# Performance work log

Hardware: AMD Instinct MI355X
Metric: run time of the kernel (lower is better)

The kernel has to match this reference:

```python
import jax, jax.numpy as jnp
import numpy as np

S, B, H, N = 512, 32, 512, 131072  # seq_len, batch, hidden_dim, num candidate spans
MAX_STEP = 20  # max_length


def setup_inputs() -> dict:
    key = jax.random.key(0)
    ks = jax.random.split(key, 8)
    hidden = jax.random.normal(ks[0], (S, B, 2 * H), dtype=jnp.float32)
    span_bids = jax.random.randint(ks[1], (N,), 0, B, dtype=jnp.int32)
    # begin in [1, S-1-MAX_STEP-1] so that begin-1>=0 and end=begin+step <= S-1
    span_begins = jax.random.randint(ks[2], (N,), 1, S - MAX_STEP - 2, dtype=jnp.int32)
    steps = jax.random.randint(ks[3], (N,), 2, MAX_STEP + 1, dtype=jnp.int32)
    span_ends = span_begins + steps
    span_flags = jax.random.randint(ks[4], (N,), 0, 2, dtype=jnp.int32)
    span_weights = jax.random.uniform(ks[5], (N,), dtype=jnp.float32)
    W1 = jax.random.normal(ks[6], (2 * H, H), dtype=jnp.float32) / np.sqrt(2.0 * H)
    b1 = jnp.zeros((H,), dtype=jnp.float32)
    W2 = jax.random.normal(ks[7], (H, 1), dtype=jnp.float32) / np.sqrt(float(H))
    b2 = jnp.zeros((1,), dtype=jnp.float32)
    return {"hidden": hidden, "span_bids": span_bids, "span_begins": span_begins,
            "span_ends": span_ends, "span_flags": span_flags, "span_weights": span_weights,
            "W1": W1, "b1": b1, "W2": W2, "b2": b2}


def reference(hidden, span_bids, span_begins, span_ends, span_flags, span_weights, W1, b1, W2, b2):
    h = W2.shape[0]  # hidden_dim
    # vectorized _span_embed: fwd diff on first half, bwd diff on second half
    fwd = hidden[span_ends - 1, span_bids, :h] - hidden[span_begins - 1, span_bids, :h]
    bwd = hidden[span_begins, span_bids, h:] - hidden[span_ends, span_bids, h:]
    feats = jnp.concatenate([fwd, bwd], axis=-1)  # [N, 2H]
    z = jnp.maximum(feats @ W1 + b1, 0.0)
    p = jax.nn.sigmoid(z @ W2 + b2)[:, 0]  # [N]
    targets = (span_flags == 1).astype(p.dtype)
    n_pos = jnp.sum(targets)
    n_tot = jnp.asarray(targets.shape[0], p.dtype)
    scale = 2.0 * n_pos / n_tot  # negative weights scaled by 2*P/(P+N)
    w_eff = jnp.where(span_flags == 1, span_weights, span_weights * scale)
    pc = jnp.clip(p, 1e-7, 1.0 - 1e-7)
    bce = -(targets * jnp.log(pc) + (1.0 - targets) * jnp.log(1.0 - pc))
    loss = jnp.mean(w_eff * bce)
    return loss
```

## Files before the change

kernel.cpp:

```cpp
#include <hip/hip_runtime.h>
#include <hip/hip_bf16.h>


typedef float f32x4 __attribute__((ext_vector_type(4)));
typedef float f32x2 __attribute__((ext_vector_type(2)));
typedef __bf16 bf16x8 __attribute__((ext_vector_type(8)));
typedef __bf16 bf16x4 __attribute__((ext_vector_type(4)));

__device__ __forceinline__ unsigned short f2bf(float f) {
  unsigned int u = __float_as_uint(f);
  u += 0x7fffu + ((u >> 16) & 1u);
  return (unsigned short)(u >> 16);
}
__device__ __forceinline__ float bf2f(unsigned int lo16) {
  return __uint_as_float(lo16 << 16);
}

__global__ void prep(const float* __restrict__ W1,
                     unsigned short* __restrict__ W1b,
                     const int* __restrict__ bids, int* __restrict__ ghist,
                     int nspans) {
  __shared__ int h[32];
  int t = threadIdx.x;
  if (blockIdx.x < 256) {
    int idx = blockIdx.x * 256 + t;
    int kc = idx & 3;
    int n  = (idx >> 2) & 511;
    int c  = idx >> 11;
    int k0 = c * 32 + kc * 8;
    unsigned short tmp[8];
#pragma unroll
    for (int j = 0; j < 8; ++j)
      tmp[j] = f2bf(W1[(k0 + j) * 512 + n]);
    *(uint4*)(W1b + c * 16384 + n * 32 + kc * 8) = *(uint4*)tmp;
  } else {
    if (t < 32) h[t] = 0;
    __syncthreads();
    int base = (blockIdx.x - 256) * 1024;
#pragma unroll
    for (int i = 0; i < 4; ++i) {
      int idx = base + t + i * 256;
      if (idx < nspans) atomicAdd(&h[bids[idx]], 1);
    }
    __syncthreads();
    if (t < 32) atomicAdd(&ghist[t], h[t]);
  }
}

__global__ void span_scatter(const int* __restrict__ bids,
                             const int* __restrict__ ghist,
                             int* __restrict__ gslot,
                             int* __restrict__ sidx, int nspans) {
  __shared__ int lh[32], lbase[32], lcur[32];
  int t = threadIdx.x;
  if (t < 32) lh[t] = 0;
  __syncthreads();
  int base = blockIdx.x * 512;
  int myb[2];
#pragma unroll
  for (int i = 0; i < 2; ++i) {
    int idx = base + t + i * 256;
    myb[i] = (idx < nspans) ? bids[idx] : -1;
    if (myb[i] >= 0) atomicAdd(&lh[myb[i]], 1);
  }
  __syncthreads();
  if (t < 32) {
    int pre = 0;
    for (int j = 0; j < t; ++j) pre += ghist[j];
    lbase[t] = pre + atomicAdd(&gslot[t], lh[t]);
    lcur[t] = 0;
  }
  __syncthreads();
#pragma unroll
  for (int i = 0; i < 2; ++i) {
    int b = myb[i];
    if (b >= 0) {
      int pos = lbase[b] + atomicAdd(&lcur[b], 1);
      sidx[pos] = base + t + i * 256;
    }
  }
}

__global__ __launch_bounds__(512, 4) void proj_gemm(
    const float* __restrict__ hidden,
    const unsigned short* __restrict__ w1b,
    unsigned char* __restrict__ Wq) {
  __shared__ __align__(16) unsigned short LB[32768];

  const int t = threadIdx.x;
  const int lane = t & 63;
  const int w = t >> 6;
  const int r0 = blockIdx.x << 6;
  const int hk = blockIdx.y << 9;
  const int q = lane >> 4;
  const int m = lane & 15;

  {
    const int kq = lane >> 4;
    const int sm = lane & 15;
#pragma unroll
    for (int ii = 0; ii < 2; ++ii) {
      const int it = (w << 1) + ii;
#pragma unroll
      for (int mt = 0; mt < 4; ++mt) {
#pragma unroll
        for (int hh = 0; hh < 2; ++hh) {
          const int kk_ = (hh << 4) + (kq << 2);
          const float* gp = hidden + ((r0 + (mt << 4) + sm) << 10)
                                   + hk + (it << 5) + kk_;
          float4 f = *(const float4*)gp;
          bf16x4 hv;
          hv[0] = (__bf16)f.x; hv[1] = (__bf16)f.y;
          hv[2] = (__bf16)f.z; hv[3] = (__bf16)f.w;
          const int qq = kk_ >> 3;
          const int kkr = kk_ & 7;
          *(bf16x4*)(LB + (((it << 2) + mt) << 9)
                        + (((qq << 4) + sm) << 3) + kkr) = hv;
        }
      }
    }
  }
  __syncthreads();

  int boffn[4];
#pragma unroll
  for (int nt = 0; nt < 4; ++nt)
    boffn[nt] = (((w << 6) + (nt << 4) + m) << 5) + (q << 3);
  const unsigned short* w1base = w1b + (blockIdx.y << 18);

  f32x4 acc[4][4];
#pragma unroll
  for (int i = 0; i < 4; ++i)
#pragma unroll
    for (int j = 0; j < 4; ++j) acc[i][j] = (f32x4){0.f, 0.f, 0.f, 0.f};

#pragma unroll
  for (int it = 0; it < 16; ++it) {
    const unsigned short* bt = w1base + (it << 14);
    bf16x8 bfr[4];
#pragma unroll
    for (int nt = 0; nt < 4; ++nt)
      bfr[nt] = *(const bf16x8*)(bt + boffn[nt]);
    bf16x8 af[4];
#pragma unroll
    for (int mt = 0; mt < 4; ++mt)
      af[mt] = *(const bf16x8*)(LB + (((it << 2) + mt) << 9)
                                   + (((q << 4) + m) << 3));
#pragma unroll
    for (int mt = 0; mt < 4; ++mt)
#pragma unroll
      for (int nt = 0; nt < 4; ++nt)
        acc[mt][nt] = __builtin_amdgcn_mfma_f32_16x16x32_bf16(af[mt], bfr[nt],
                                                              acc[mt][nt], 0, 0, 0);
  }

  {
    const int cb = (w << 6) + (m << 2);
#pragma unroll
    for (int mt = 0; mt < 4; ++mt) {
#pragma unroll
      for (int r = 0; r < 4; ++r) {
        unsigned int o = __builtin_amdgcn_cvt_pk_fp8_f32(
            acc[mt][0][r], acc[mt][1][r], 0, false);
        o = __builtin_amdgcn_cvt_pk_fp8_f32(
            acc[mt][2][r], acc[mt][3][r], o, true);
        int grow = r0 + (mt << 4) + (q << 2) + r;
        if (hk == 0) {
          *(unsigned int*)(Wq + (grow << 10) + cb) = o;
        } else if (grow >= 32) {
          *(unsigned int*)(Wq + ((grow - 32) << 10) + 512 + cb) = o;
        }
      }
    }
  }
}

#define SPB 64
__global__ __launch_bounds__(256) void span_eval(
    const unsigned char* __restrict__ Wq,
    const int* __restrict__ sidx,
    const int* __restrict__ bids, const int* __restrict__ begins,
    const int* __restrict__ ends, const int* __restrict__ flags,
    const float* __restrict__ weights,
    const float* __restrict__ b1, const float* __restrict__ w2,
    const float* __restrict__ b2, float* __restrict__ partials) {
  __shared__ int oB[SPB], oE[SPB], sfl[SPB];
  __shared__ float swt[SPB];
  __shared__ float red[4][3];
  const int t = threadIdx.x;
  const int lane = t & 63;
  const int w = t >> 6;
  const int h = lane >> 5;
  const int hl = lane & 31;

  const int nblk = gridDim.x;
  int lb = blockIdx.x;
  if ((nblk & 7) == 0) {
    const int cpx = nblk >> 3;
    lb = (blockIdx.x & 7) * cpx + (blockIdx.x >> 3);
  }
  const int sbase = lb * SPB;

  if (t < SPB) {
    int s = sidx[sbase + t];
    int b = bids[s], bg = begins[s], en = ends[s];
    oB[t] = (((bg - 1) << 5) + b) << 10;
    oE[t] = (((en - 1) << 5) + b) << 10;
    sfl[t] = flags[s];
    swt[t] = weights[s];
  }
  __syncthreads();

  const int sp0 = ((w << 1) + h) << 3;
  const int c0 = hl << 4;
  f32x2 b1p[8], w2p[8];
#pragma unroll
  for (int i = 0; i < 8; ++i) {
#pragma unroll
    for (int j2 = 0; j2 < 2; ++j2) {
      int j = 2 * i + j2;
      int colp = ((hl >> 2) << 6) + ((j & 3) << 4) + ((hl & 3) << 2) + (j >> 2);
      b1p[i][j2] = b1[colp];
      w2p[i][j2] = w2[colp];
    }
  }

  auto dec2 = [](unsigned int v, f32x2* f) {
    f[0] = __builtin_amdgcn_cvt_pk_f32_fp8(v, false);
    f[1] = __builtin_amdgcn_cvt_pk_f32_fp8(v, true);
  };

  uint4 BU[4], BV[4], EU[4], EV[4];
  auto ld = [&](int slot, int j) {
    int ob = oB[sp0 + j], oe = oE[sp0 + j];
    BU[slot] = *(const uint4*)(Wq + ob + c0);
    BV[slot] = *(const uint4*)(Wq + ob + 512 + c0);
    EU[slot] = *(const uint4*)(Wq + oe + c0);
    EV[slot] = *(const uint4*)(Wq + oe + 512 + c0);
  };
  ld(0, 0); ld(1, 1); ld(2, 2); ld(3, 3);

  const f32x2 zero2 = (f32x2){0.f, 0.f};
  float mylogit = 0.f;
#pragma unroll
  for (int j = 0; j < 8; ++j) {
    const int slot = j & 3;
    f32x2 bu2[8], bv2[8], eu2[8], ev2[8];
    dec2(BU[slot].x, bu2 + 0); dec2(BU[slot].y, bu2 + 2);
    dec2(BU[slot].z, bu2 + 4); dec2(BU[slot].w, bu2 + 6);
    dec2(BV[slot].x, bv2 + 0); dec2(BV[slot].y, bv2 + 2);
    dec2(BV[slot].z, bv2 + 4); dec2(BV[slot].w, bv2 + 6);
    dec2(EU[slot].x, eu2 + 0); dec2(EU[slot].y, eu2 + 2);
    dec2(EU[slot].z, eu2 + 4); dec2(EU[slot].w, eu2 + 6);
    dec2(EV[slot].x, ev2 + 0); dec2(EV[slot].y, ev2 + 2);
    dec2(EV[slot].z, ev2 + 4); dec2(EV[slot].w, ev2 + 6);
    if (j + 4 < 8) ld(slot, j + 4);
    f32x2 sv2 = zero2;
#pragma unroll
    for (int i = 0; i < 8; ++i) {
      f32x2 zp = eu2[i] - bu2[i] + bv2[i] - ev2[i] + b1p[i];
      zp = __builtin_elementwise_max(zp, zero2);
      sv2 = sv2 + zp * w2p[i];
    }
    float sv = sv2[0] + sv2[1];
    sv += __shfl_xor(sv, 1);
    sv += __shfl_xor(sv, 2);
    sv += __shfl_xor(sv, 4);
    sv += __shfl_xor(sv, 8);
    sv += __shfl_xor(sv, 16);
    if (hl == j) mylogit = sv;
  }

  mylogit = __shfl(mylogit, ((lane & 8) << 2) + (lane & 7));

  float pos_t = 0.f, neg_t = 0.f, cnt_t = 0.f;
  if (lane < 16) {
    int sl = (w << 4) + lane;
    float logit = mylogit + b2[0];
    float p = 1.f / (1.f + expf(-logit));
    p = fminf(fmaxf(p, 1e-7f), 1.f - 1e-7f);
    int fl = sfl[sl];
    float bce = (fl == 1) ? -logf(p) : -logf(1.f - p);
    float term = swt[sl] * bce;
    pos_t = (fl == 1) ? term : 0.f;
    neg_t = (fl == 1) ? 0.f : term;
    cnt_t = (fl == 1) ? 1.f : 0.f;
  }
#pragma unroll
  for (int off = 1; off < 64; off <<= 1) {
    pos_t += __shfl_xor(pos_t, off);
    neg_t += __shfl_xor(neg_t, off);
    cnt_t += __shfl_xor(cnt_t, off);
  }
  if (lane == 0) { red[w][0] = pos_t; red[w][1] = neg_t; red[w][2] = cnt_t; }
  __syncthreads();
  if (t == 0) {
    partials[(blockIdx.x << 2) + 0] = red[0][0] + red[1][0] + red[2][0] + red[3][0];
    partials[(blockIdx.x << 2) + 1] = red[0][1] + red[1][1] + red[2][1] + red[3][1];
    partials[(blockIdx.x << 2) + 2] = red[0][2] + red[1][2] + red[2][2] + red[3][2];
  }
}

__global__ void finalize(const float* __restrict__ parts, int nblk,
                         float* __restrict__ out, int nspans) {
  __shared__ float sp[4], sn[4], sc[4];
  float P = 0.f, Ng = 0.f, C = 0.f;
  for (int i = threadIdx.x; i < nblk; i += 256) {
    P += parts[(i << 2) + 0];
    Ng += parts[(i << 2) + 1];
    C += parts[(i << 2) + 2];
  }
#pragma unroll
  for (int off = 1; off < 64; off <<= 1) {
    P += __shfl_xor(P, off);
    Ng += __shfl_xor(Ng, off);
    C += __shfl_xor(C, off);
  }
  int w = threadIdx.x >> 6;
  if ((threadIdx.x & 63) == 0) { sp[w] = P; sn[w] = Ng; sc[w] = C; }
  __syncthreads();
  if (threadIdx.x == 0) {
    P = sp[0] + sp[1] + sp[2] + sp[3];
    Ng = sn[0] + sn[1] + sn[2] + sn[3];
    C = sc[0] + sc[1] + sc[2] + sc[3];
    float scale = 2.f * C / (float)nspans;
    out[0] = (P + scale * Ng) / (float)nspans;
  }
}

extern "C" void kernel_launch(void* const* d_in, const int* in_sizes, int n_in,
                              void* d_out, int out_size, void* d_ws, size_t ws_size,
                              hipStream_t stream) {
  const float* hidden = (const float*)d_in[0];
  const int* bids     = (const int*)d_in[1];
  const int* begins   = (const int*)d_in[2];
  const int* ends     = (const int*)d_in[3];
  const int* flags    = (const int*)d_in[4];
  const float* weights = (const float*)d_in[5];
  const float* W1 = (const float*)d_in[6];
  const float* b1 = (const float*)d_in[7];
  const float* W2 = (const float*)d_in[8];
  const float* b2 = (const float*)d_in[9];
  float* out = (float*)d_out;
  const int nspans = in_sizes[1];
  const int nblk = nspans / SPB;

  float* partials = (float*)d_ws;
  unsigned short* W1b = (unsigned short*)((char*)d_ws + (1 << 18));
  unsigned char* Wq = (unsigned char*)((char*)d_ws + (2 << 20));
  int* ghist = (int*)((char*)d_ws + (19 << 20));
  int* gslot = ghist + 32;
  int* sidx  = (int*)((char*)d_ws + (20 << 20));

  hipMemsetAsync(ghist, 0, 64 * sizeof(int), stream);
  prep<<<384, 256, 0, stream>>>(W1, W1b, bids, ghist, nspans);
  span_scatter<<<(nspans + 511) / 512, 256, 0, stream>>>(bids, ghist, gslot,
                                                         sidx, nspans);
  proj_gemm<<<dim3(256, 2), 512, 0, stream>>>(hidden, W1b, Wq);
  span_eval<<<nblk, 256, 0, stream>>>(Wq, sidx, bids, begins, ends, flags,
                                      weights, b1, W2, b2, partials);
  finalize<<<1, 256, 0, stream>>>(partials, nblk, out, nspans);
}
```

Baseline: 166.2 us.

## Process four span chunks per block with double-buffered span metadata

span_eval now loops over four 64-span chunks per block instead of one, so the grid shrinks fourfold. The per-span setup (b1/w2 loads, b2 read, the block reduction and partial write) is amortised across the chunks. Metadata for the next chunk is loaded into a second shared buffer while the current chunk's gathers run. This cuts per-block overhead and the finalize input size, at the cost of fewer blocks to hide gather latency and an extra barrier per chunk.

```diff
diff --git a/kernel.cpp b/kernel.cpp
--- a/kernel.cpp
+++ b/kernel.cpp
@@ -176,6 +176,7 @@
 }
 
 #define SPB 64
+#define CHUNKS 4
 __global__ __launch_bounds__(256) void span_eval(
     const unsigned char* __restrict__ Wq,
     const int* __restrict__ sidx,
@@ -184,8 +185,8 @@
     const float* __restrict__ weights,
     const float* __restrict__ b1, const float* __restrict__ w2,
     const float* __restrict__ b2, float* __restrict__ partials) {
-  __shared__ int oB[SPB], oE[SPB], sfl[SPB];
-  __shared__ float swt[SPB];
+  __shared__ int oB[2][SPB], oE[2][SPB], sfl[2][SPB];
+  __shared__ float swt[2][SPB];
   __shared__ float red[4][3];
   const int t = threadIdx.x;
   const int lane = t & 63;
@@ -199,17 +200,20 @@
     const int cpx = nblk >> 3;
     lb = (blockIdx.x & 7) * cpx + (blockIdx.x >> 3);
   }
-  const int sbase = lb * SPB;
-
-  if (t < SPB) {
-    int s = sidx[sbase + t];
-    int b = bids[s], bg = begins[s], en = ends[s];
-    oB[t] = (((bg - 1) << 5) + b) << 10;
-    oE[t] = (((en - 1) << 5) + b) << 10;
-    sfl[t] = flags[s];
-    swt[t] = weights[s];
-  }
-  __syncthreads();
+  const int base0 = lb * (SPB * CHUNKS);
+
+  auto ldmeta = [&](int c) {
+    if (t < SPB) {
+      int s = sidx[base0 + c * SPB + t];
+      int b = bids[s], bg = begins[s], en = ends[s];
+      int p = c & 1;
+      oB[p][t] = (((bg - 1) << 5) + b) << 10;
+      oE[p][t] = (((en - 1) << 5) + b) << 10;
+      sfl[p][t] = flags[s];
+      swt[p][t] = weights[s];
+    }
+  };
+  ldmeta(0);
 
   const int sp0 = ((w << 1) + h) << 3;
   const int c0 = hl << 4;
@@ -224,68 +228,77 @@
       w2p[i][j2] = w2[colp];
     }
   }
+  const float b2v = b2[0];
+  __syncthreads();
 
   auto dec2 = [](unsigned int v, f32x2* f) {
     f[0] = __builtin_amdgcn_cvt_pk_f32_fp8(v, false);
     f[1] = __builtin_amdgcn_cvt_pk_f32_fp8(v, true);
   };
 
-  uint4 BU[4], BV[4], EU[4], EV[4];
-  auto ld = [&](int slot, int j) {
-    int ob = oB[sp0 + j], oe = oE[sp0 + j];
-    BU[slot] = *(const uint4*)(Wq + ob + c0);
-    BV[slot] = *(const uint4*)(Wq + ob + 512 + c0);
-    EU[slot] = *(const uint4*)(Wq + oe + c0);
-    EV[slot] = *(const uint4*)(Wq + oe + 512 + c0);
-  };
-  ld(0, 0); ld(1, 1); ld(2, 2); ld(3, 3);
-
   const f32x2 zero2 = (f32x2){0.f, 0.f};
-  float mylogit = 0.f;
-#pragma unroll
-  for (int j = 0; j < 8; ++j) {
-    const int slot = j & 3;
-    f32x2 bu2[8], bv2[8], eu2[8], ev2[8];
-    dec2(BU[slot].x, bu2 + 0); dec2(BU[slot].y, bu2 + 2);
-    dec2(BU[slot].z, bu2 + 4); dec2(BU[slot].w, bu2 + 6);
-    dec2(BV[slot].x, bv2 + 0); dec2(BV[slot].y, bv2 + 2);
-    dec2(BV[slot].z, bv2 + 4); dec2(BV[slot].w, bv2 + 6);
-    dec2(EU[slot].x, eu2 + 0); dec2(EU[slot].y, eu2 + 2);
-    dec2(EU[slot].z, eu2 + 4); dec2(EU[slot].w, eu2 + 6);
-    dec2(EV[slot].x, ev2 + 0); dec2(EV[slot].y, ev2 + 2);
-    dec2(EV[slot].z, ev2 + 4); dec2(EV[slot].w, ev2 + 6);
-    if (j + 4 < 8) ld(slot, j + 4);
-    f32x2 sv2 = zero2;
-#pragma unroll
-    for (int i = 0; i < 8; ++i) {
-      f32x2 zp = eu2[i] - bu2[i] + bv2[i] - ev2[i] + b1p[i];
-      zp = __builtin_elementwise_max(zp, zero2);
-      sv2 = sv2 + zp * w2p[i];
-    }
-    float sv = sv2[0] + sv2[1];
-    sv += __shfl_xor(sv, 1);
-    sv += __shfl_xor(sv, 2);
-    sv += __shfl_xor(sv, 4);
-    sv += __shfl_xor(sv, 8);
-    sv += __shfl_xor(sv, 16);
-    if (hl == j) mylogit = sv;
-  }
-
-  mylogit = __shfl(mylogit, ((lane & 8) << 2) + (lane & 7));
-
   float pos_t = 0.f, neg_t = 0.f, cnt_t = 0.f;
-  if (lane < 16) {
-    int sl = (w << 4) + lane;
-    float logit = mylogit + b2[0];
-    float p = 1.f / (1.f + expf(-logit));
-    p = fminf(fmaxf(p, 1e-7f), 1.f - 1e-7f);
-    int fl = sfl[sl];
-    float bce = (fl == 1) ? -logf(p) : -logf(1.f - p);
-    float term = swt[sl] * bce;
-    pos_t = (fl == 1) ? term : 0.f;
-    neg_t = (fl == 1) ? 0.f : term;
-    cnt_t = (fl == 1) ? 1.f : 0.f;
-  }
+
+  for (int c = 0; c < CHUNKS; ++c) {
+    const int cur = c & 1;
+    uint4 BU[4], BV[4], EU[4], EV[4];
+    auto ld = [&](int slot, int j) {
+      int ob = oB[cur][sp0 + j], oe = oE[cur][sp0 + j];
+      BU[slot] = *(const uint4*)(Wq + ob + c0);
+      BV[slot] = *(const uint4*)(Wq + ob + 512 + c0);
+      EU[slot] = *(const uint4*)(Wq + oe + c0);
+      EV[slot] = *(const uint4*)(Wq + oe + 512 + c0);
+    };
+    ld(0, 0); ld(1, 1); ld(2, 2); ld(3, 3);
+    if (c + 1 < CHUNKS) ldmeta(c + 1);
+
+    float mylogit = 0.f;
+#pragma unroll
+    for (int j = 0; j < 8; ++j) {
+      const int slot = j & 3;
+      f32x2 bu2[8], bv2[8], eu2[8], ev2[8];
+      dec2(BU[slot].x, bu2 + 0); dec2(BU[slot].y, bu2 + 2);
+      dec2(BU[slot].z, bu2 + 4); dec2(BU[slot].w, bu2 + 6);
+      dec2(BV[slot].x, bv2 + 0); dec2(BV[slot].y, bv2 + 2);
+      dec2(BV[slot].z, bv2 + 4); dec2(BV[slot].w, bv2 + 6);
+      dec2(EU[slot].x, eu2 + 0); dec2(EU[slot].y, eu2 + 2);
+      dec2(EU[slot].z, eu2 + 4); dec2(EU[slot].w, eu2 + 6);
+      dec2(EV[slot].x, ev2 + 0); dec2(EV[slot].y, ev2 + 2);
+      dec2(EV[slot].z, ev2 + 4); dec2(EV[slot].w, ev2 + 6);
+      if (j + 4 < 8) ld(slot, j + 4);
+      f32x2 sv2 = zero2;
+#pragma unroll
+      for (int i = 0; i < 8; ++i) {
+        f32x2 zp = eu2[i] - bu2[i] + bv2[i] - ev2[i] + b1p[i];
+        zp = __builtin_elementwise_max(zp, zero2);
+        sv2 = sv2 + zp * w2p[i];
+      }
+      float sv = sv2[0] + sv2[1];
+      sv += __shfl_xor(sv, 1);
+      sv += __shfl_xor(sv, 2);
+      sv += __shfl_xor(sv, 4);
+      sv += __shfl_xor(sv, 8);
+      sv += __shfl_xor(sv, 16);
+      if (hl == j) mylogit = sv;
+    }
+
+    mylogit = __shfl(mylogit, ((lane & 8) << 2) + (lane & 7));
+
+    if (lane < 16) {
+      int sl = (w << 4) + lane;
+      float logit = mylogit + b2v;
+      float p = 1.f / (1.f + expf(-logit));
+      p = fminf(fmaxf(p, 1e-7f), 1.f - 1e-7f);
+      int fl = sfl[cur][sl];
+      float bce = (fl == 1) ? -logf(p) : -logf(1.f - p);
+      float term = swt[cur][sl] * bce;
+      pos_t += (fl == 1) ? term : 0.f;
+      neg_t += (fl == 1) ? 0.f : term;
+      cnt_t += (fl == 1) ? 1.f : 0.f;
+    }
+    __syncthreads();
+  }
+
 #pragma unroll
   for (int off = 1; off < 64; off <<= 1) {
     pos_t += __shfl_xor(pos_t, off);
@@ -343,7 +356,7 @@
   const float* b2 = (const float*)d_in[9];
   float* out = (float*)d_out;
   const int nspans = in_sizes[1];
-  const int nblk = nspans / SPB;
+  const int nblk = nspans / (SPB * CHUNKS);
 
   float* partials = (float*)d_ws;
   unsigned short* W1b = (unsigned short*)((char*)d_ws + (1 << 18));
```

After: 163.0 us. No clear change (-1.9%).
